# Kernel optimization log

Hardware: AMD Instinct MI355X
Metric: run time of the kernel (lower is better)

Reference implementation:

```python
import jax, jax.numpy as jnp
import numpy as np

STRIDE = 1
PADDING = 1
DILATION = 1


def setup_inputs() -> dict:
    key = jax.random.key(0)
    k1, k2, k3 = jax.random.split(key, 3)
    b_i, b_j, c, h, w = 32, 1, 128, 32, 32
    oc, kh, kw = 128, 3, 3
    x = jax.random.normal(k1, (b_i, b_j, c, h, w), dtype=jnp.float32)
    weight = jax.random.normal(k2, (b_i, oc, c, kh, kw), dtype=jnp.float32) * 0.05
    bias = jax.random.normal(k3, (b_i, b_j, oc), dtype=jnp.float32) * 0.05
    return {"x": x, "weight": weight, "bias": bias}


def reference(x, weight, bias):
    # x: [b_i, b_j, c, h, w]; weight: [b_i, oc, c, kh, kw]; bias: [b_i, b_j, oc]
    b_i, b_j, c, h, w = x.shape
    oc, kh, kw = weight.shape[1], weight.shape[3], weight.shape[4]
    # fold per-sample dim into channels, run one grouped conv with groups=b_i
    xr = jnp.transpose(x, (1, 0, 2, 3, 4)).reshape(b_j, b_i * c, h, w)
    wr = weight.reshape(b_i * oc, c, kh, kw)
    out = jax.lax.conv_general_dilated(
        xr, wr,
        window_strides=(STRIDE, STRIDE),
        padding=[(PADDING, PADDING), (PADDING, PADDING)],
        rhs_dilation=(DILATION, DILATION),
        dimension_numbers=("NCHW", "OIHW", "NCHW"),
        feature_group_count=b_i,
    )  # [b_j, b_i*oc, H, W]
    H, W = out.shape[-2], out.shape[-1]
    out = out.reshape(b_j, b_i, oc, H, W).transpose(1, 0, 2, 3, 4)  # [b_i, b_j, oc, H, W]
    out = out + bias[:, :, :, None, None]
    return out
```

## Files before the change

kernel.cpp:

```cpp
#include <hip/hip_runtime.h>

typedef unsigned short u16;
typedef unsigned int u32;
typedef __attribute__((ext_vector_type(2))) unsigned int u32x2;
typedef __attribute__((ext_vector_type(8))) short bf16x8;
typedef __attribute__((ext_vector_type(4))) float f32x4;

#define CIN 128
#define OC 128
#define NP 1024
#define KTOT 1152
#define NSTEP 18
#define BK 64
#define TILE_U16 8192
#define SAMP_U16 (NSTEP * TILE_U16)

typedef const u32 __attribute__((address_space(1)))* gptr_t;
typedef u32 __attribute__((address_space(3)))* lptr_t;

__device__ __forceinline__ u16 f2bf(float f) {
  unsigned b = __builtin_bit_cast(unsigned, f);
  b += 0x7fffu + ((b >> 16) & 1u);
  return (u16)(b >> 16);
}

__global__ void wcvt_kernel(const float* __restrict__ w, u16* __restrict__ wbf2) {
  __shared__ u16 lds[KTOT];
  const int blk = blockIdx.x;
  const int t = threadIdx.x;
  const int i = blk >> 7, row = blk & 127;
  const float* src = w + (size_t)blk * KTOT;
#pragma unroll
  for (int e = 0; e < 9; ++e) {
    int idx = t + 128 * e;
    lds[idx] = f2bf(src[idx]);
  }
  __syncthreads();
  u16* dst = wbf2 + (size_t)i * SAMP_U16;
  const int rsw = row & 7;
#pragma unroll
  for (int e = 0; e < 9; ++e) {
    const int o = t + 128 * e;
    const int s = o >> 6;
    const int slotk = (o >> 3) & 7;
    const int ee = o & 7;
    dst[s * TILE_U16 + (row * 8 + (slotk ^ rsw)) * 8 + ee] = lds[t * 9 + e];
  }
}

__global__ __launch_bounds__(512, 1) void conv_mfma(
    const float* __restrict__ x,
    const u16* __restrict__ wbf2,
    const float* __restrict__ bias,
    float* __restrict__ out) {
  __shared__ u16 Xs[6 * 34 * 128];
  __shared__ u16 Asw[4][TILE_U16];

  const int wg = (int)blockIdx.x;
  const int swz = (wg & 7) * 32 + (wg >> 3);
  const int i  = swz >> 3;
  const int pt = swz & 7;
  const int p0 = pt * 128;
  const int tid = (int)threadIdx.x;
  const int lane = tid & 63;
  const int wid = tid >> 6;
  const int wm = wid >> 2;
  const int wn = wid & 3;
  const int lcol = lane & 15;
  const int lhi  = lane >> 4;

  const float* xi = x + (size_t)i * CIN * NP;
  const u16*   wt = wbf2 + (size_t)i * SAMP_U16;

#define STAGE(step) do {                                               \
    const char* _tb = (const char*)(wt + (step) * TILE_U16);           \
    char* _lb = (char*)&Asw[(step) & 3][0];                            \
    _Pragma("unroll")                                                  \
    for (int _j = 0; _j < 2; ++_j) {                                   \
      const int _off = wid * 2048 + _j * 1024;                         \
      __builtin_amdgcn_global_load_lds(                                \
          (gptr_t)(_tb + _off + lane * 16),                            \
          (lptr_t)(_lb + _off), 16, 0, 0);                             \
    }                                                                  \
  } while (0)

  STAGE(0);
  STAGE(1);

  {
    const int xx = tid & 31;
    const int cg = (tid >> 5) & 7;
    const int rh = tid >> 8;
    const int col = xx + 1;
    const int csw = col & 7;
#pragma unroll
    for (int rr = 0; rr < 3; ++rr) {
      const int r = rh * 3 + rr;
      const int yr = 4 * pt - 1 + r;
      float v[16];
      if ((unsigned)yr < 32u) {
        const float* src = xi + (size_t)(cg * 16) * NP + yr * 32 + xx;
#pragma unroll
        for (int j = 0; j < 16; ++j) v[j] = src[(size_t)j * NP];
      } else {
#pragma unroll
        for (int j = 0; j < 16; ++j) v[j] = 0.f;
      }
      u32 pk[8];
#pragma unroll
      for (int m = 0; m < 8; ++m)
        pk[m] = (u32)f2bf(v[2 * m]) | ((u32)f2bf(v[2 * m + 1]) << 16);
#pragma unroll
      for (int q = 0; q < 4; ++q) {
        const int cslot = cg * 2 + (q >> 1);
        const int idx = ((r * 34 + col) * 16 + (cslot ^ csw)) * 8 + (q & 1) * 4;
        *(u32x2*)(&Xs[idx]) = (u32x2){pk[2 * q], pk[2 * q + 1]};
      }
    }
    if (tid < 192) {
      const int r = tid / 32;
      const int hc = ((tid >> 4) & 1) ? 33 : 0;
      const int s = tid & 15;
      const int idx = ((r * 34 + hc) * 16 + (s ^ (hc & 7))) * 8;
      *(bf16x8*)(&Xs[idx]) = (bf16x8){0, 0, 0, 0, 0, 0, 0, 0};
    }
  }

  f32x4 acc[4][2];
#pragma unroll
  for (int mi = 0; mi < 4; ++mi)
#pragma unroll
    for (int ni = 0; ni < 2; ++ni)
      acc[mi][ni] = (f32x4){0.f, 0.f, 0.f, 0.f};

  __syncthreads();

#pragma unroll
  for (int step = 0; step < NSTEP; ++step) {
    const int buf = step & 3;
    const int rs = step >> 1;
    const int r3 = rs / 3;
    const int dy = r3 - 1;
    const int dx = (rs - r3 * 3) - 1;
    const int c0s = (step & 1) * 8;

    if (step + 2 < NSTEP) STAGE(step + 2);

    if (step + 2 < NSTEP) {
      asm volatile("s_waitcnt vmcnt(4)" ::: "memory");
    } else if (step + 1 < NSTEP) {
      asm volatile("s_waitcnt vmcnt(2)" ::: "memory");
    } else {
      asm volatile("s_waitcnt vmcnt(0)" ::: "memory");
    }
    __builtin_amdgcn_s_barrier();
    __builtin_amdgcn_sched_barrier(0);

    bf16x8 af[2][4], bfr[2][2];
#pragma unroll
    for (int kkk = 0; kkk < 2; ++kkk) {
#pragma unroll
      for (int mi = 0; mi < 4; ++mi) {
        const int row = wm * 64 + mi * 16 + lcol;
        const int slot = (kkk * 4 + lhi) ^ (row & 7);
        af[kkk][mi] = *(const bf16x8*)(&Asw[buf][row * BK + slot * 8]);
      }
#pragma unroll
      for (int ni = 0; ni < 2; ++ni) {
        const int srow = wn + 1 + dy;
        const int col  = ni * 16 + lcol + 1 + dx;
        const int cslot = c0s + kkk * 4 + lhi;
        const int idx = ((srow * 34 + col) * 16 + (cslot ^ (col & 7))) * 8;
        bfr[kkk][ni] = *(const bf16x8*)(&Xs[idx]);
      }
    }
    __builtin_amdgcn_s_setprio(1);
#pragma unroll
    for (int kkk = 0; kkk < 2; ++kkk)
#pragma unroll
      for (int mi = 0; mi < 4; ++mi)
#pragma unroll
        for (int ni = 0; ni < 2; ++ni)
          acc[mi][ni] = __builtin_amdgcn_mfma_f32_16x16x32_bf16(
              af[kkk][mi], bfr[kkk][ni], acc[mi][ni], 0, 0, 0);
    __builtin_amdgcn_s_setprio(0);
    __builtin_amdgcn_s_barrier();
  }

  const int row0 = lhi * 4;
#pragma unroll
  for (int mi = 0; mi < 4; ++mi) {
    const int oc = wm * 64 + mi * 16 + row0;
#pragma unroll
    for (int jj = 0; jj < 4; ++jj) {
      const float bv = bias[i * OC + oc + jj];
      float* orow = out + ((size_t)i * OC + oc + jj) * NP;
#pragma unroll
      for (int ni = 0; ni < 2; ++ni) {
        const int pg = p0 + wn * 32 + ni * 16 + lcol;
        orow[pg] = acc[mi][ni][jj] + bv;
      }
    }
  }
#undef STAGE
}

extern "C" void kernel_launch(void* const* d_in, const int* in_sizes, int n_in,
                              void* d_out, int out_size, void* d_ws, size_t ws_size,
                              hipStream_t stream) {
  const float* x    = (const float*)d_in[0];
  const float* w    = (const float*)d_in[1];
  const float* bias = (const float*)d_in[2];
  float* out = (float*)d_out;
  u16* wbf2 = (u16*)d_ws;

  wcvt_kernel<<<dim3(32 * OC), dim3(128), 0, stream>>>(w, wbf2);
  conv_mfma<<<dim3(256), dim3(512), 0, stream>>>(x, wbf2, bias, out);
}
```

Baseline: 30.64 us.

## Pre-convert input to padded bf16 in prep kernel and shrink conv tiles

Moves the fp32-to-bf16 conversion and padding of x out of the conv kernel into a fused prep kernel (alongside the weight conversion), writing a zero-padded swizzled bf16 layout to workspace. The conv kernel then loads its input halo with async global_load_lds instead of doing register-side conversion. It also halves the per-block tile (256 threads, 64 pixels, 2 blocks per CU, double-buffered weights) and restructures the wait/barrier placement. In exchange it adds a memset and extra global traffic for the bf16 x copy, plus a shallower weight prefetch pipeline.

```diff
diff --git a/kernel.cpp b/kernel.cpp
--- a/kernel.cpp
+++ b/kernel.cpp
@@ -2,7 +2,7 @@
 
 typedef unsigned short u16;
 typedef unsigned int u32;
-typedef __attribute__((ext_vector_type(2))) unsigned int u32x2;
+typedef __attribute__((ext_vector_type(4))) unsigned int u32x4;
 typedef __attribute__((ext_vector_type(8))) short bf16x8;
 typedef __attribute__((ext_vector_type(4))) float f32x4;
 
@@ -14,6 +14,9 @@
 #define BK 64
 #define TILE_U16 8192
 #define SAMP_U16 (NSTEP * TILE_U16)
+#define XROW_U16 (36 * 128)
+#define XSAMP_U16 (34 * XROW_U16)
+#define XBF_BYTES ((size_t)32 * XSAMP_U16 * 2)
 
 typedef const u32 __attribute__((address_space(1)))* gptr_t;
 typedef u32 __attribute__((address_space(3)))* lptr_t;
@@ -24,108 +27,104 @@
   return (u16)(b >> 16);
 }
 
-__global__ void wcvt_kernel(const float* __restrict__ w, u16* __restrict__ wbf2) {
-  __shared__ u16 lds[KTOT];
+__global__ void prep_kernel(const float* __restrict__ w,
+                            const float* __restrict__ x,
+                            u16* __restrict__ wbf2,
+                            u16* __restrict__ xbf) {
   const int blk = blockIdx.x;
   const int t = threadIdx.x;
-  const int i = blk >> 7, row = blk & 127;
-  const float* src = w + (size_t)blk * KTOT;
-#pragma unroll
-  for (int e = 0; e < 9; ++e) {
-    int idx = t + 128 * e;
-    lds[idx] = f2bf(src[idx]);
-  }
-  __syncthreads();
-  u16* dst = wbf2 + (size_t)i * SAMP_U16;
-  const int rsw = row & 7;
-#pragma unroll
-  for (int e = 0; e < 9; ++e) {
-    const int o = t + 128 * e;
-    const int s = o >> 6;
-    const int slotk = (o >> 3) & 7;
-    const int ee = o & 7;
-    dst[s * TILE_U16 + (row * 8 + (slotk ^ rsw)) * 8 + ee] = lds[t * 9 + e];
-  }
-}
-
-__global__ __launch_bounds__(512, 1) void conv_mfma(
-    const float* __restrict__ x,
+  if (blk < 4096) {
+    __shared__ u16 lds[KTOT];
+    const int i = blk >> 7, row = blk & 127;
+    const float* src = w + (size_t)blk * KTOT;
+#pragma unroll
+    for (int e = 0; e < 9; ++e) {
+      int idx = t + 128 * e;
+      lds[idx] = f2bf(src[idx]);
+    }
+    __syncthreads();
+    u16* dst = wbf2 + (size_t)i * SAMP_U16;
+    const int rsw = row & 7;
+#pragma unroll
+    for (int e = 0; e < 9; ++e) {
+      const int o = t + 128 * e;
+      const int s = o >> 6;
+      const int slotk = (o >> 3) & 7;
+      const int ee = o & 7;
+      dst[s * TILE_U16 + (row * 8 + (slotk ^ rsw)) * 8 + ee] = lds[t * 9 + e];
+    }
+  } else {
+    const int b = blk - 4096;
+    const int i = b >> 5, y = b & 31;
+    const int xx = t & 31;
+    const int cg2 = t >> 5;
+    const float* src = x + ((size_t)(i * CIN + cg2 * 32) * 32 + y) * 32 + xx;
+    float v[32];
+#pragma unroll
+    for (int j = 0; j < 32; ++j) v[j] = src[(size_t)j * NP];
+    u32 pk[16];
+#pragma unroll
+    for (int m = 0; m < 16; ++m)
+      pk[m] = (u32)f2bf(v[2 * m]) | ((u32)f2bf(v[2 * m + 1]) << 16);
+    const int col = xx + 1;
+    u16* rowp = xbf + (size_t)(i * 34 + (y + 1)) * XROW_U16 + col * 128;
+#pragma unroll
+    for (int h = 0; h < 4; ++h) {
+      const int sl = (cg2 * 4 + h) ^ (col & 7);
+      *(u32x4*)(rowp + sl * 8) =
+          (u32x4){pk[h * 4], pk[h * 4 + 1], pk[h * 4 + 2], pk[h * 4 + 3]};
+    }
+  }
+}
+
+__global__ __launch_bounds__(256, 2) void conv_mfma(
+    const u16* __restrict__ xbf,
     const u16* __restrict__ wbf2,
     const float* __restrict__ bias,
     float* __restrict__ out) {
-  __shared__ u16 Xs[6 * 34 * 128];
-  __shared__ u16 Asw[4][TILE_U16];
+  __shared__ u16 Xs[4 * 36 * 128];
+  __shared__ u16 Asw[2][TILE_U16];
 
   const int wg = (int)blockIdx.x;
-  const int swz = (wg & 7) * 32 + (wg >> 3);
-  const int i  = swz >> 3;
-  const int pt = swz & 7;
-  const int p0 = pt * 128;
+  const int swz = (wg & 7) * 64 + (wg >> 3);
+  const int i  = swz >> 4;
+  const int pt = swz & 15;
+  const int p0 = pt * 64;
   const int tid = (int)threadIdx.x;
   const int lane = tid & 63;
   const int wid = tid >> 6;
-  const int wm = wid >> 2;
-  const int wn = wid & 3;
+  const int wm = wid >> 1;
+  const int wn = wid & 1;
   const int lcol = lane & 15;
   const int lhi  = lane >> 4;
 
-  const float* xi = x + (size_t)i * CIN * NP;
-  const u16*   wt = wbf2 + (size_t)i * SAMP_U16;
+  const u16* wt = wbf2 + (size_t)i * SAMP_U16;
+  const u16* xsrc = xbf + (size_t)(i * 34 + 2 * pt) * XROW_U16;
 
 #define STAGE(step) do {                                               \
     const char* _tb = (const char*)(wt + (step) * TILE_U16);           \
-    char* _lb = (char*)&Asw[(step) & 3][0];                            \
+    char* _lb = (char*)&Asw[(step) & 1][0];                            \
     _Pragma("unroll")                                                  \
-    for (int _j = 0; _j < 2; ++_j) {                                   \
-      const int _off = wid * 2048 + _j * 1024;                         \
+    for (int _r = 0; _r < 4; ++_r) {                                   \
+      const int _off = _r * 4096 + tid * 16;                           \
       __builtin_amdgcn_global_load_lds(                                \
-          (gptr_t)(_tb + _off + lane * 16),                            \
-          (lptr_t)(_lb + _off), 16, 0, 0);                             \
+          (gptr_t)(_tb + _off), (lptr_t)(_lb + _off), 16, 0, 0);       \
     }                                                                  \
   } while (0)
 
+  {
+    const char* _xs = (const char*)xsrc;
+    char* _xl = (char*)&Xs[0];
+#pragma unroll
+    for (int r = 0; r < 9; ++r) {
+      const int off = r * 4096 + tid * 16;
+      __builtin_amdgcn_global_load_lds((gptr_t)(_xs + off),
+                                       (lptr_t)(_xl + off), 16, 0, 0);
+    }
+  }
   STAGE(0);
   STAGE(1);
 
-  {
-    const int xx = tid & 31;
-    const int cg = (tid >> 5) & 7;
-    const int rh = tid >> 8;
-    const int col = xx + 1;
-    const int csw = col & 7;
-#pragma unroll
-    for (int rr = 0; rr < 3; ++rr) {
-      const int r = rh * 3 + rr;
-      const int yr = 4 * pt - 1 + r;
-      float v[16];
-      if ((unsigned)yr < 32u) {
-        const float* src = xi + (size_t)(cg * 16) * NP + yr * 32 + xx;
-#pragma unroll
-        for (int j = 0; j < 16; ++j) v[j] = src[(size_t)j * NP];
-      } else {
-#pragma unroll
-        for (int j = 0; j < 16; ++j) v[j] = 0.f;
-      }
-      u32 pk[8];
-#pragma unroll
-      for (int m = 0; m < 8; ++m)
-        pk[m] = (u32)f2bf(v[2 * m]) | ((u32)f2bf(v[2 * m + 1]) << 16);
-#pragma unroll
-      for (int q = 0; q < 4; ++q) {
-        const int cslot = cg * 2 + (q >> 1);
-        const int idx = ((r * 34 + col) * 16 + (cslot ^ csw)) * 8 + (q & 1) * 4;
-        *(u32x2*)(&Xs[idx]) = (u32x2){pk[2 * q], pk[2 * q + 1]};
-      }
-    }
-    if (tid < 192) {
-      const int r = tid / 32;
-      const int hc = ((tid >> 4) & 1) ? 33 : 0;
-      const int s = tid & 15;
-      const int idx = ((r * 34 + hc) * 16 + (s ^ (hc & 7))) * 8;
-      *(bf16x8*)(&Xs[idx]) = (bf16x8){0, 0, 0, 0, 0, 0, 0, 0};
-    }
-  }
-
   f32x4 acc[4][2];
 #pragma unroll
   for (int mi = 0; mi < 4; ++mi)
@@ -133,29 +132,19 @@
     for (int ni = 0; ni < 2; ++ni)
       acc[mi][ni] = (f32x4){0.f, 0.f, 0.f, 0.f};
 
-  __syncthreads();
+  asm volatile("s_waitcnt vmcnt(4)" ::: "memory");
+  __builtin_amdgcn_s_barrier();
+  __builtin_amdgcn_sched_barrier(0);
 
 #pragma unroll
   for (int step = 0; step < NSTEP; ++step) {
-    const int buf = step & 3;
+    const int buf = step & 1;
     const int rs = step >> 1;
     const int r3 = rs / 3;
     const int dy = r3 - 1;
     const int dx = (rs - r3 * 3) - 1;
     const int c0s = (step & 1) * 8;
 
-    if (step + 2 < NSTEP) STAGE(step + 2);
-
-    if (step + 2 < NSTEP) {
-      asm volatile("s_waitcnt vmcnt(4)" ::: "memory");
-    } else if (step + 1 < NSTEP) {
-      asm volatile("s_waitcnt vmcnt(2)" ::: "memory");
-    } else {
-      asm volatile("s_waitcnt vmcnt(0)" ::: "memory");
-    }
-    __builtin_amdgcn_s_barrier();
-    __builtin_amdgcn_sched_barrier(0);
-
     bf16x8 af[2][4], bfr[2][2];
 #pragma unroll
     for (int kkk = 0; kkk < 2; ++kkk) {
@@ -170,7 +159,7 @@
         const int srow = wn + 1 + dy;
         const int col  = ni * 16 + lcol + 1 + dx;
         const int cslot = c0s + kkk * 4 + lhi;
-        const int idx = ((srow * 34 + col) * 16 + (cslot ^ (col & 7))) * 8;
+        const int idx = ((srow * 36 + col) * 16 + (cslot ^ (col & 7))) * 8;
         bfr[kkk][ni] = *(const bf16x8*)(&Xs[idx]);
       }
     }
@@ -184,7 +173,13 @@
           acc[mi][ni] = __builtin_amdgcn_mfma_f32_16x16x32_bf16(
               af[kkk][mi], bfr[kkk][ni], acc[mi][ni], 0, 0, 0);
     __builtin_amdgcn_s_setprio(0);
-    __builtin_amdgcn_s_barrier();
+
+    if (step + 1 < NSTEP) {
+      asm volatile("s_waitcnt vmcnt(0)" ::: "memory");
+      __builtin_amdgcn_s_barrier();
+      __builtin_amdgcn_sched_barrier(0);
+      if (step + 2 < NSTEP) STAGE(step + 2);
+    }
   }
 
   const int row0 = lhi * 4;
@@ -213,7 +208,9 @@
   const float* bias = (const float*)d_in[2];
   float* out = (float*)d_out;
   u16* wbf2 = (u16*)d_ws;
-
-  wcvt_kernel<<<dim3(32 * OC), dim3(128), 0, stream>>>(w, wbf2);
-  conv_mfma<<<dim3(256), dim3(512), 0, stream>>>(x, wbf2, bias, out);
-}
+  u16* xbf  = (u16*)((char*)d_ws + (16u << 20));
+
+  hipMemsetAsync(xbf, 0, XBF_BYTES, stream);
+  prep_kernel<<<dim3(5120), dim3(128), 0, stream>>>(w, x, wbf2, xbf);
+  conv_mfma<<<dim3(512), dim3(256), 0, stream>>>(xbf, wbf2, bias, out);
+}
```

After: 39.65 us. +29.4%, slower.
